# Kernel optimization log

Measured on AMD Instinct MI355X. Metric: run time of the kernel, lower is better.

The kernel has to match this reference:

```python
import jax, jax.numpy as jnp
import numpy as np

# dims: S slots, B batch, D pred-rep dim, E slot-embedding dim, H hidden/output dim, V per-slot vocab
S, B, D, E, H, V = 7, 4096, 1024, 128, 512, 200
D0 = D + E  # layer-0 LSTM input size


def setup_inputs() -> dict:
    key = jax.random.key(0)
    ks = jax.random.split(key, 12)
    rn = lambda k, shape, s=0.02: jax.random.normal(k, shape, jnp.float32) * s
    return {
        "pred_reps": jax.random.normal(ks[0], (B, D), jnp.float32),
        "slot_labels": jax.random.randint(ks[1], (S, B), 0, V),
        "emb": rn(ks[2], (S, V, E), 1.0),
        # layer 0: per-slot LSTMCell + highway params
        "Wih0": rn(ks[3], (S, 4 * H, D0)), "Whh0": rn(ks[4], (S, 4 * H, H)),
        "bih0": jnp.zeros((S, 4 * H), jnp.float32), "bhh0": jnp.zeros((S, 4 * H), jnp.float32),
        "hwW0": rn(ks[5], (S, H, D0 + H)), "hwb0": jnp.zeros((S, H), jnp.float32),
        "linW0": rn(ks[6], (S, H, D0)),
        # layer 1 (input size = H)
        "Wih1": rn(ks[7], (S, 4 * H, H)), "Whh1": rn(ks[8], (S, 4 * H, H)),
        "bih1": jnp.zeros((S, 4 * H), jnp.float32), "bhh1": jnp.zeros((S, 4 * H), jnp.float32),
        "hwW1": rn(ks[9], (S, H, 2 * H)), "hwb1": jnp.zeros((S, H), jnp.float32),
        "linW1": rn(ks[10], (S, H, H)),
    }


def _lstm_cell(x, h, c, Wih, Whh, bih, bhh):
    # torch LSTMCell: gates ordered i, f, g, o
    gates = x @ Wih.T + bih + h @ Whh.T + bhh
    i, f, g, o = jnp.split(gates, 4, axis=-1)
    c_new = jax.nn.sigmoid(f) * c + jax.nn.sigmoid(i) * jnp.tanh(g)
    h_new = jax.nn.sigmoid(o) * jnp.tanh(c_new)
    return h_new, c_new


def reference(pred_reps, slot_labels, emb, Wih0, Whh0, bih0, bhh0, hwW0, hwb0, linW0,
              Wih1, Whh1, bih1, bhh1, hwW1, hwb1, linW1):
    def step(carry, xs):
        h0, c0, h1, c1 = carry
        (tbl, idx, wih0, whh0, bi0, bh0, hw0, hb0, lw0,
         wih1, whh1, bi1, bh1, hw1, hb1, lw1) = xs
        # per-slot embedding gather + concat with predicate reps  -> [B, D0]
        x = jnp.concatenate([pred_reps, tbl[idx]], axis=-1)
        # layer 0 cell + highway gate
        h0n, c0n = _lstm_cell(x, h0, c0, wih0, whh0, bi0, bh0)
        gate0 = jax.nn.sigmoid(jnp.concatenate([x, h0n], axis=-1) @ hw0.T + hb0)
        x1 = gate0 * h0n + (1.0 - gate0) * (x @ lw0.T)
        # layer 1 cell (its highway output is dead code in the original: curr_input
        # after the last layer is discarded, so we skip it -- same math)
        h1n, c1n = _lstm_cell(x1, h1, c1, wih1, whh1, bi1, bh1)
        return (h0n, c0n, h1n, c1n), None

    init = tuple(jnp.zeros((B, H), pred_reps.dtype) for _ in range(4))
    xs = (emb, slot_labels, Wih0, Whh0, bih0, bhh0, hwW0, hwb0, linW0,
          Wih1, Whh1, bih1, bhh1, hwW1, hwb1, linW1)
    carry, _ = jax.lax.scan(step, init, xs)
    return carry[2]  # last_h: top-layer hidden after final slot
```

## Files before the change

kernel.cpp:

```cpp
#include <hip/hip_runtime.h>
#include <stdint.h>

typedef unsigned short u16;

#define S_   7
#define B_   4096
#define D_   1024
#define E_   128
#define H_   512
#define V_   200
#define D0_  1152
#define K0_  1664
#define KX1  1024
#define G4H  2048
#define XW   2048
#define X1W  2048

typedef __bf16 bf16x8 __attribute__((ext_vector_type(8)));
typedef float  f32x4  __attribute__((ext_vector_type(4)));
typedef u16    u16x8  __attribute__((ext_vector_type(8)));

__device__ __forceinline__ u16 f2bf(float f) {
  union { float f; uint32_t u; } v; v.f = f;
  uint32_t r = v.u + 0x7fffu + ((v.u >> 16) & 1u);
  return (u16)(r >> 16);
}
__device__ __forceinline__ float bf2f(u16 b) {
  union { uint32_t u; float f; } v; v.u = ((uint32_t)b) << 16;
  return v.f;
}
__device__ __forceinline__ float sigmoidf_(float x) { return 1.0f / (1.0f + __expf(-x)); }
__device__ __forceinline__ float tanhf_(float x) {
  float t = __expf(-2.f * fabsf(x));
  return copysignf((1.f - t) / (1.f + t), x);
}

__device__ __forceinline__ void glds16(const u16* g, u16* l) {
  __builtin_amdgcn_global_load_lds(
      (const __attribute__((address_space(1))) uint32_t*)g,
      (__attribute__((address_space(3))) uint32_t*)l, 16, 0, 0);
}

__device__ __forceinline__ void cvt8s(const float* src, u16* dst) {
  const float4* p = (const float4*)src;
  float4 x = p[0], y = p[1];
  u16x8 o;
  o[0]=f2bf(x.x); o[1]=f2bf(x.y); o[2]=f2bf(x.z); o[3]=f2bf(x.w);
  o[4]=f2bf(y.x); o[5]=f2bf(y.y); o[6]=f2bf(y.z); o[7]=f2bf(y.w);
  *(u16x8*)dst = o;
}

__device__ __forceinline__ void pk_gates(const float* __restrict__ Wih,
                                         const float* __restrict__ Whh,
                                         u16* __restrict__ dst,
                                         int idx, int stride, int NG, int KK,
                                         int P1, int P2, int KA, int KB) {
  #pragma unroll
  for (int u = 0; u < 4; ++u) {
    int i = idx + u * stride;
    int r = i / NG, kg = i - r * NG;
    int k8 = kg * 8;
    int g = r >> 9, j = r & 511;
    long drow = (j >> 4) * 64 + g * 16 + (j & 15);
    const float* sp = (k8 < P1) ? Wih + (long)r * KA + k8
                    : (k8 < P2) ? Whh + (long)r * KB + (k8 - P1)
                                : Wih + (long)r * KA + P1 + (k8 - P2);
    cvt8s(sp, &dst[drow * KK + k8]);
  }
}
__device__ __forceinline__ void pk_hw(const float* __restrict__ src,
                                      u16* __restrict__ dst,
                                      int idx, int stride, int off16, int KS, bool Z2) {
  #pragma unroll
  for (int u = 0; u < 4; ++u) {
    int i = idx + u * stride;
    int r = i / 208, kg = i - r * 208;
    int k8 = kg * 8;
    long drow = ((r & 511) >> 4) * 32 + off16 + (r & 15);
    u16* d = &dst[drow * K0_ + k8];
    if (Z2 && k8 >= 1024 && k8 < 1536) {
      u16x8 z = {};
      *(u16x8*)d = z;
    } else {
      const float* sp = (k8 < 1024) ? src + (long)r * KS + k8
                      : (k8 < 1536) ? src + (long)r * KS + 1152 + (k8 - 1024)
                                    : src + (long)r * KS + 1024 + (k8 - 1536);
      cvt8s(sp, d);
    }
  }
}

__global__ void pack_predz4(const float* __restrict__ pred, u16* __restrict__ dst) {
  const int NG = XW / 8;
  const int stride = gridDim.x * 256;
  int idx = blockIdx.x * 256 + threadIdx.x;
  #pragma unroll
  for (int u = 0; u < 4; ++u) {
    int i = idx + u * stride;
    int row = i / NG, kg = i - row * NG;
    int k8 = kg * 8;
    u16* d = &dst[(long)row * XW + k8];
    if (k8 < 1024) {
      cvt8s(pred + (long)row * D_ + k8, d);
    } else {
      u16x8 z = {};
      *(u16x8*)d = z;
    }
  }
}

__global__ void xgather(const float* __restrict__ emb, const int* __restrict__ labels,
                        u16* __restrict__ EMB) {
  int b = blockIdx.x;
  int e = threadIdx.x;
  #pragma unroll
  for (int s = 0; s < S_; ++s) {
    int ix = labels[s * B_ + b];
    EMB[((long)(s * B_ + b)) * E_ + e] = f2bf(emb[((long)(s * V_ + ix)) * E_ + e]);
  }
}

__global__ void bias_sum(const float* __restrict__ a, const float* __restrict__ b,
                         float* __restrict__ o, int n) {
  int i = blockIdx.x * 256 + threadIdx.x;
  if (i < n) o[i] = a[i] + b[i];
}
__global__ void zero_f(float* __restrict__ p, int n) {
  for (int i = blockIdx.x * 256 + threadIdx.x; i < n; i += gridDim.x * 256) p[i] = 0.f;
}
__global__ void zero_u16k(u16* __restrict__ p, int n) {
  for (int i = blockIdx.x * 256 + threadIdx.x; i < n; i += gridDim.x * 256) p[i] = 0;
}

struct GemmP {
  const u16 *r0, *r1, *r2, *W;
  const float *bsum;
  float *cbuf;
  u16 *hdst;
  float *hf32;
  const u16 *h0src;
  int ld0, ld1, ld2, t1, t2, ldw, nt, ntn, tnw_sh, ncc_sh, tmw, hld, hoff, h0ld, mode;
};
struct PackP {
  const float *wih0, *whh0, *wih1, *whh1, *hww, *linw;
  u16 *wc0, *wc1, *whl;
};

__global__ __launch_bounds__(256, 4)
void gemm_multi(GemmP pa, GemmP pb, GemmP pc, PackP pk, int nA, int nAB, int nABC) {
  const int b   = blockIdx.x;
  const int tid = threadIdx.x;

  if (b >= nABC) {
    int rb = b - nABC;
    if (rb < 416) {
      pk_gates(pk.wih0, pk.whh0, pk.wc0, rb * 256 + tid, 416 * 256,
               208, K0_, 1024, 1536, D0_, H_);
    } else if (rb < 672) {
      pk_gates(pk.wih1, pk.whh1, pk.wc1, (rb - 416) * 256 + tid, 256 * 256,
               128, KX1, 512, 1024, H_, H_);
    } else {
      int sb = rb - 672;
      if (sb < 104) pk_hw(pk.hww,  pk.whl, sb * 256 + tid,        104 * 256, 0,  K0_, false);
      else          pk_hw(pk.linw, pk.whl, (sb - 104) * 256 + tid, 104 * 256, 16, D0_, true);
    }
    return;
  }

  __shared__ __align__(16) u16 lds[4 * 4096];
  GemmP P = pc; int base = nAB;
  if (b < nAB) { P = pb; base = nA; }
  if (b < nA)  { P = pa; base = 0; }
  const int bidx = b - base;

  u16* lA = lds;
  u16* lW = lds + 2 * 4096;
  const int lane = tid & 63;
  const int wave = tid >> 6;
  const int xcd = bidx & 7, ci = bidx >> 3;
  const int tn = ((xcd & ((1 << P.ncc_sh) - 1)) << P.tnw_sh) | (ci & ((1 << P.tnw_sh) - 1));
  const int tm = (xcd >> P.ncc_sh) * P.tmw + (ci >> P.tnw_sh);
  const long row0 = (long)tm * 128;
  const long col0 = (long)tn * 128;
  const int wm = (wave >> 1) * 64;
  const int wn = (wave & 1) * 64;
  const int fr = lane & 15;
  const int hi = lane >> 4;

  const int s_row = wave * 16 + (lane >> 2);
  const int scol = ((lane & 3) ^ ((lane >> 3) & 3)) * 8;
  const u16* gr0 = P.r0 + (row0 + s_row) * (long)P.ld0 + scol;
  const u16* gr1 = P.r1 + (row0 + s_row) * (long)P.ld1 + scol;
  const u16* gr2 = P.r2 + (row0 + s_row) * (long)P.ld2 + scol;
  const u16* gw  = P.W  + (col0 + s_row) * (long)P.ldw + scol;
  const int dst0 = wave * 512 + lane * 8;

  auto stage = [&](int t, int buf) {
    const u16* g; long ld;
    if (t < P.t1)      { g = gr0 + (long)t * 32;          ld = P.ld0; }
    else if (t < P.t2) { g = gr1 + (long)(t - P.t1) * 32; ld = P.ld1; }
    else               { g = gr2 + (long)(t - P.t2) * 32; ld = P.ld2; }
    const u16* gww = gw + (long)t * 32;
    u16* dA = lA + buf * 4096 + dst0;
    u16* dW = lW + buf * 4096 + dst0;
    glds16(g,           dA);
    glds16(g + 64 * ld, dA + 2048);
    glds16(gww,                      dW);
    glds16(gww + 64 * (long)P.ldw,   dW + 2048);
  };

  const int koff = (hi ^ ((fr >> 1) & 3)) * 8;
  int aoff[4], woff[4];
  #pragma unroll
  for (int m = 0; m < 4; ++m) aoff[m] = (wm + m * 16 + fr) * 32 + koff;
  #pragma unroll
  for (int n = 0; n < 4; ++n) woff[n] = (wn + n * 16 + fr) * 32 + koff;

  f32x4 acc[4][4] = {};
  const int nt = P.nt;

  stage(0, 0);

  for (int t = 0; t < nt; ++t) {
    __syncthreads();
    if (t + 1 < nt) stage(t + 1, (t + 1) & 1);
    const u16* Ab = lA + (t & 1) * 4096;
    const u16* Wb = lW + (t & 1) * 4096;
    bf16x8 af[4], wf[4];
    #pragma unroll
    for (int m = 0; m < 4; ++m) af[m] = *(const bf16x8*)&Ab[aoff[m]];
    #pragma unroll
    for (int n = 0; n < 4; ++n) wf[n] = *(const bf16x8*)&Wb[woff[n]];
    #pragma unroll
    for (int m = 0; m < 4; ++m)
      #pragma unroll
      for (int n = 0; n < 4; ++n)
        acc[m][n] = __builtin_amdgcn_mfma_f32_16x16x32_bf16(af[m], wf[n], acc[m][n], 0, 0, 0);
  }

  const int cr = (lane >> 4) * 4;
  const int jg = wn >> 6;

  if (P.mode == 0) {
    const int j = tn * 32 + jg * 16 + fr;
    const float bi = P.bsum[j], bf = P.bsum[512 + j];
    const float bg = P.bsum[1024 + j], bo = P.bsum[1536 + j];
    #pragma unroll
    for (int m = 0; m < 4; ++m) {
      const long rbase = row0 + wm + m * 16 + cr;
      #pragma unroll
      for (int r = 0; r < 4; ++r) {
        const long ri = rbase + r;
        float gi = acc[m][0][r] + bi;
        float gf = acc[m][1][r] + bf;
        float gg = acc[m][2][r] + bg;
        float go = acc[m][3][r] + bo;
        float cv = P.cbuf[ri * H_ + j];
        float cn = sigmoidf_(gf) * cv + sigmoidf_(gi) * tanhf_(gg);
        float hn = sigmoidf_(go) * tanhf_(cn);
        P.cbuf[ri * H_ + j] = cn;
        P.hdst[ri * P.hld + P.hoff + j] = f2bf(hn);
        if (P.hf32) P.hf32[ri * H_ + j] = hn;
      }
    }
  } else {
    #pragma unroll
    for (int pp = 0; pp < 2; ++pp) {
      const int j = tn * 64 + jg * 32 + pp * 16 + fr;
      const float bj = P.bsum[j];
      #pragma unroll
      for (int m = 0; m < 4; ++m) {
        const long rbase = row0 + wm + m * 16 + cr;
        #pragma unroll
        for (int r = 0; r < 4; ++r) {
          const long ri = rbase + r;
          float gv = sigmoidf_(acc[m][2 * pp][r] + bj);
          float h0 = bf2f(P.h0src[ri * (long)P.h0ld + j]);
          float x1 = gv * h0 + (1.f - gv) * acc[m][2 * pp + 1][r];
          P.hdst[ri * P.hld + P.hoff + j] = f2bf(x1);
        }
      }
    }
  }
}

extern "C" void kernel_launch(void* const* d_in, const int* in_sizes, int n_in,
                              void* d_out, int out_size, void* d_ws, size_t ws_size,
                              hipStream_t stream) {
  const float* pred   = (const float*)d_in[0];
  const int*   labels = (const int*)d_in[1];
  const float* emb    = (const float*)d_in[2];
  const float* Wih0   = (const float*)d_in[3];
  const float* Whh0   = (const float*)d_in[4];
  const float* bih0   = (const float*)d_in[5];
  const float* bhh0   = (const float*)d_in[6];
  const float* hwW0   = (const float*)d_in[7];
  const float* hwb0   = (const float*)d_in[8];
  const float* linW0  = (const float*)d_in[9];
  const float* Wih1   = (const float*)d_in[10];
  const float* Whh1   = (const float*)d_in[11];
  const float* bih1   = (const float*)d_in[12];
  const float* bhh1   = (const float*)d_in[13];
  float* out = (float*)d_out;

  char* ws = (char*)d_ws;
  size_t off = 0;
  auto alloc = [&](size_t bytes) {
    char* p = ws + off;
    off = (off + bytes + 255) & ~(size_t)255;
    return p;
  };
  u16* WC0   = (u16*)alloc((size_t)S_ * G4H * K0_ * 2);
  u16* WHLw  = (u16*)alloc((size_t)S_ * 1024 * K0_ * 2);
  u16* WC1   = (u16*)alloc((size_t)S_ * G4H * KX1 * 2);
  u16* xcat  = (u16*)alloc((size_t)B_ * XW * 2);
  u16* EMB   = (u16*)alloc((size_t)S_ * B_ * E_ * 2);
  u16* x1cat = (u16*)alloc((size_t)B_ * X1W * 2);
  float* c0   = (float*)alloc((size_t)B_ * H_ * 4);
  float* c1   = (float*)alloc((size_t)B_ * H_ * 4);
  float* bs0  = (float*)alloc((size_t)S_ * G4H * 4);
  float* bs1  = (float*)alloc((size_t)S_ * G4H * 4);

  auto mkPk = [&](int s) {
    PackP K;
    K.wih0 = Wih0 + (size_t)s * G4H * D0_;
    K.whh0 = Whh0 + (size_t)s * G4H * H_;
    K.wih1 = Wih1 + (size_t)s * G4H * H_;
    K.whh1 = Whh1 + (size_t)s * G4H * H_;
    K.hww  = hwW0 + (size_t)s * H_ * K0_;
    K.linw = linW0 + (size_t)s * H_ * D0_;
    K.wc0  = WC0  + (size_t)s * G4H * K0_;
    K.wc1  = WC1  + (size_t)s * G4H * KX1;
    K.whl  = WHLw + (size_t)s * 1024 * K0_;
    return K;
  };

  GemmP z = {};
  gemm_multi<<<880, 256, 0, stream>>>(z, z, z, mkPk(0), 0, 0, 0);
  pack_predz4<<<1024, 256, 0, stream>>>(pred, xcat);
  xgather<<<B_, E_, 0, stream>>>(emb, labels, EMB);
  bias_sum<<<56, 256, 0, stream>>>(bih0, bhh0, bs0, S_ * G4H);
  bias_sum<<<56, 256, 0, stream>>>(bih1, bhh1, bs1, S_ * G4H);
  zero_f<<<256, 256, 0, stream>>>(c0, B_ * H_);
  zero_f<<<256, 256, 0, stream>>>(c1, B_ * H_);
  zero_u16k<<<2048, 256, 0, stream>>>(x1cat, B_ * X1W);

  auto mkA = [&](int s) {
    GemmP P;
    P.r0 = xcat;                               P.ld0 = XW;  P.t1 = 32;
    P.r1 = xcat + 1024 + ((s + 1) & 1) * 512;  P.ld1 = XW;  P.t2 = 48;
    P.r2 = EMB + (size_t)s * B_ * E_;          P.ld2 = E_;
    P.W = WC0 + (size_t)s * G4H * K0_;         P.ldw = K0_; P.nt = 52;
    P.ntn = 16; P.tnw_sh = 3; P.ncc_sh = 1; P.tmw = 8;
    P.bsum = bs0 + (size_t)s * G4H; P.cbuf = c0;
    P.hdst = xcat; P.hld = XW; P.hoff = 1024 + (s & 1) * 512;
    P.hf32 = nullptr; P.h0src = xcat; P.h0ld = 0; P.mode = 0;
    return P;
  };
  auto mkB = [&](int s) {
    GemmP P;
    P.r0 = xcat;                               P.ld0 = XW;  P.t1 = 32;
    P.r1 = xcat + 1024 + (s & 1) * 512;        P.ld1 = XW;  P.t2 = 48;
    P.r2 = EMB + (size_t)s * B_ * E_;          P.ld2 = E_;
    P.W = WHLw + (size_t)s * 1024 * K0_;       P.ldw = K0_; P.nt = 52;
    P.ntn = 8; P.tnw_sh = 2; P.ncc_sh = 1; P.tmw = 8;
    P.bsum = hwb0 + (size_t)s * H_; P.cbuf = nullptr;
    P.hdst = x1cat; P.hld = X1W; P.hoff = (s & 1) * 512;
    P.hf32 = nullptr;
    P.h0src = xcat + 1024 + (s & 1) * 512; P.h0ld = XW; P.mode = 1;
    return P;
  };
  auto mkC = [&](int s) {
    GemmP P;
    P.r0 = x1cat + (s & 1) * 512;              P.ld0 = X1W; P.t1 = 16;
    P.r1 = x1cat + 1024 + ((s + 1) & 1) * 512; P.ld1 = X1W; P.t2 = 32;
    P.r2 = P.r0;                               P.ld2 = X1W;
    P.W = WC1 + (size_t)s * G4H * KX1;         P.ldw = KX1; P.nt = 32;
    P.ntn = 16; P.tnw_sh = 3; P.ncc_sh = 1; P.tmw = 8;
    P.bsum = bs1 + (size_t)s * G4H; P.cbuf = c1;
    P.hdst = x1cat; P.hld = X1W; P.hoff = 1024 + (s & 1) * 512;
    P.hf32 = (s == 6) ? out : nullptr; P.h0src = x1cat; P.h0ld = 0; P.mode = 0;
    return P;
  };

  for (int k = 0; k <= 8; ++k) {
    const int nA = (k <= 6) ? 512 : 0;
    const int nB = (k >= 1 && k <= 7) ? 256 : 0;
    const int nC = (k >= 2) ? 512 : 0;
    const int nD = (k <= 5) ? 880 : 0;
    GemmP pa, pb, pc;
    if (nA) pa = mkA(k);
    if (nB) pb = mkB(k - 1);
    if (nC) pc = mkC(k - 2);
    GemmP any = nA ? pa : (nB ? pb : pc);
    if (!nA) pa = any;
    if (!nB) pb = any;
    if (!nC) pc = any;
    PackP pk = mkPk(nD ? (k + 1) : 0);
    gemm_multi<<<nA + nB + nC + nD, 256, 0, stream>>>(pa, pb, pc, pk,
                                                      nA, nA + nB, nA + nB + nC);
  }
}
```

Before: 657.2 us.

## Enlarge GEMM tiles to 256x128 with BK=64 and triple-buffered LDS pipeline

The fused GEMM kernel moves to 512-thread blocks, each computing a 256x128 output tile with a K step of 64 instead of 32. LDS now holds three buffers, and the mainloop uses explicit vmcnt waits so two stages stay in flight. MFMA issue is wrapped in s_setprio. The aim is more data reuse per LDS load and fewer barriers per K-element. The cost is a large LDS footprint (about 147KB per block), which probably limits each CU to one resident block and lowers occupancy. Grid sizes and the weight-pack block partitioning are rescaled to match.

```diff
diff --git a/kernel.cpp b/kernel.cpp
--- a/kernel.cpp
+++ b/kernel.cpp
@@ -146,96 +146,114 @@
   u16 *wc0, *wc1, *whl;
 };
 
-__global__ __launch_bounds__(256, 4)
+__global__ __launch_bounds__(512, 2)
 void gemm_multi(GemmP pa, GemmP pb, GemmP pc, PackP pk, int nA, int nAB, int nABC) {
   const int b   = blockIdx.x;
   const int tid = threadIdx.x;
 
   if (b >= nABC) {
     int rb = b - nABC;
-    if (rb < 416) {
-      pk_gates(pk.wih0, pk.whh0, pk.wc0, rb * 256 + tid, 416 * 256,
+    if (rb < 208) {
+      pk_gates(pk.wih0, pk.whh0, pk.wc0, rb * 512 + tid, 208 * 512,
                208, K0_, 1024, 1536, D0_, H_);
-    } else if (rb < 672) {
-      pk_gates(pk.wih1, pk.whh1, pk.wc1, (rb - 416) * 256 + tid, 256 * 256,
+    } else if (rb < 336) {
+      pk_gates(pk.wih1, pk.whh1, pk.wc1, (rb - 208) * 512 + tid, 128 * 512,
                128, KX1, 512, 1024, H_, H_);
+    } else if (rb < 388) {
+      pk_hw(pk.hww,  pk.whl, (rb - 336) * 512 + tid, 52 * 512, 0,  K0_, false);
     } else {
-      int sb = rb - 672;
-      if (sb < 104) pk_hw(pk.hww,  pk.whl, sb * 256 + tid,        104 * 256, 0,  K0_, false);
-      else          pk_hw(pk.linw, pk.whl, (sb - 104) * 256 + tid, 104 * 256, 16, D0_, true);
+      pk_hw(pk.linw, pk.whl, (rb - 388) * 512 + tid, 52 * 512, 16, D0_, true);
     }
     return;
   }
 
-  __shared__ __align__(16) u16 lds[4 * 4096];
+  __shared__ __align__(16) u16 lds[3 * 16384 + 3 * 8192];
+  u16* lA = lds;
+  u16* lW = lds + 3 * 16384;
+
   GemmP P = pc; int base = nAB;
   if (b < nAB) { P = pb; base = nA; }
   if (b < nA)  { P = pa; base = 0; }
   const int bidx = b - base;
 
-  u16* lA = lds;
-  u16* lW = lds + 2 * 4096;
   const int lane = tid & 63;
   const int wave = tid >> 6;
   const int xcd = bidx & 7, ci = bidx >> 3;
   const int tn = ((xcd & ((1 << P.ncc_sh) - 1)) << P.tnw_sh) | (ci & ((1 << P.tnw_sh) - 1));
   const int tm = (xcd >> P.ncc_sh) * P.tmw + (ci >> P.tnw_sh);
-  const long row0 = (long)tm * 128;
+  const long row0 = (long)tm * 256;
   const long col0 = (long)tn * 128;
   const int wm = (wave >> 1) * 64;
   const int wn = (wave & 1) * 64;
   const int fr = lane & 15;
-  const int hi = lane >> 4;
-
-  const int s_row = wave * 16 + (lane >> 2);
-  const int scol = ((lane & 3) ^ ((lane >> 3) & 3)) * 8;
-  const u16* gr0 = P.r0 + (row0 + s_row) * (long)P.ld0 + scol;
-  const u16* gr1 = P.r1 + (row0 + s_row) * (long)P.ld1 + scol;
-  const u16* gr2 = P.r2 + (row0 + s_row) * (long)P.ld2 + scol;
-  const u16* gw  = P.W  + (col0 + s_row) * (long)P.ldw + scol;
+  const int fk = (lane >> 4) * 8;
+
+  const int srow = wave * 8 + (lane >> 3);
+  const int scol = ((lane & 7) ^ ((lane >> 3) & 7)) * 8;
+  const u16* gr0 = P.r0 + (row0 + srow) * (long)P.ld0 + scol;
+  const u16* gr1 = P.r1 + (row0 + srow) * (long)P.ld1 + scol;
+  const u16* gr2 = P.r2 + (row0 + srow) * (long)P.ld2 + scol;
+  const u16* gw  = P.W  + (col0 + srow) * (long)P.ldw + scol;
   const int dst0 = wave * 512 + lane * 8;
 
   auto stage = [&](int t, int buf) {
     const u16* g; long ld;
-    if (t < P.t1)      { g = gr0 + (long)t * 32;          ld = P.ld0; }
-    else if (t < P.t2) { g = gr1 + (long)(t - P.t1) * 32; ld = P.ld1; }
-    else               { g = gr2 + (long)(t - P.t2) * 32; ld = P.ld2; }
-    const u16* gww = gw + (long)t * 32;
-    u16* dA = lA + buf * 4096 + dst0;
-    u16* dW = lW + buf * 4096 + dst0;
-    glds16(g,           dA);
-    glds16(g + 64 * ld, dA + 2048);
-    glds16(gww,                      dW);
-    glds16(gww + 64 * (long)P.ldw,   dW + 2048);
-  };
-
-  const int koff = (hi ^ ((fr >> 1) & 3)) * 8;
+    if (t < P.t1)      { g = gr0 + (long)t * 64;          ld = P.ld0; }
+    else if (t < P.t2) { g = gr1 + (long)(t - P.t1) * 64; ld = P.ld1; }
+    else               { g = gr2 + (long)(t - P.t2) * 64; ld = P.ld2; }
+    const u16* gww = gw + (long)t * 64;
+    u16* dA = lA + buf * 16384 + dst0;
+    u16* dW = lW + buf * 8192 + dst0;
+    #pragma unroll
+    for (int i = 0; i < 4; ++i) glds16(g + (long)(i * 64) * ld, dA + i * 4096);
+    #pragma unroll
+    for (int j2 = 0; j2 < 2; ++j2) glds16(gww + (long)(j2 * 64) * P.ldw, dW + j2 * 4096);
+  };
+
   int aoff[4], woff[4];
   #pragma unroll
-  for (int m = 0; m < 4; ++m) aoff[m] = (wm + m * 16 + fr) * 32 + koff;
-  #pragma unroll
-  for (int n = 0; n < 4; ++n) woff[n] = (wn + n * 16 + fr) * 32 + koff;
+  for (int m = 0; m < 4; ++m) aoff[m] = (wm + m * 16 + fr) * 64;
+  #pragma unroll
+  for (int n = 0; n < 4; ++n) woff[n] = (wn + n * 16 + fr) * 64;
+  const int swz = (fr & 7) << 3;
+  const int kk0 = (0 + fk) ^ swz;
+  const int kk1 = (32 + fk) ^ swz;
 
   f32x4 acc[4][4] = {};
   const int nt = P.nt;
 
   stage(0, 0);
+  stage(1, 1);
 
   for (int t = 0; t < nt; ++t) {
-    __syncthreads();
-    if (t + 1 < nt) stage(t + 1, (t + 1) & 1);
-    const u16* Ab = lA + (t & 1) * 4096;
-    const u16* Wb = lW + (t & 1) * 4096;
-    bf16x8 af[4], wf[4];
-    #pragma unroll
-    for (int m = 0; m < 4; ++m) af[m] = *(const bf16x8*)&Ab[aoff[m]];
-    #pragma unroll
-    for (int n = 0; n < 4; ++n) wf[n] = *(const bf16x8*)&Wb[woff[n]];
+    if (t + 1 < nt) asm volatile("s_waitcnt vmcnt(6)\n\ts_barrier" ::: "memory");
+    else            asm volatile("s_waitcnt vmcnt(0)\n\ts_barrier" ::: "memory");
+    if (t + 2 < nt) stage(t + 2, (t + 2) % 3);
+
+    const u16* Ab = lA + (t % 3) * 16384;
+    const u16* Wb = lW + (t % 3) * 8192;
+    bf16x8 af0[4], wf0[4], af1[4], wf1[4];
+    #pragma unroll
+    for (int m = 0; m < 4; ++m) af0[m] = *(const bf16x8*)&Ab[aoff[m] + kk0];
+    #pragma unroll
+    for (int n = 0; n < 4; ++n) wf0[n] = *(const bf16x8*)&Wb[woff[n] + kk0];
+    #pragma unroll
+    for (int m = 0; m < 4; ++m) af1[m] = *(const bf16x8*)&Ab[aoff[m] + kk1];
+    #pragma unroll
+    for (int n = 0; n < 4; ++n) wf1[n] = *(const bf16x8*)&Wb[woff[n] + kk1];
+
+    __builtin_amdgcn_s_setprio(1);
     #pragma unroll
     for (int m = 0; m < 4; ++m)
       #pragma unroll
       for (int n = 0; n < 4; ++n)
-        acc[m][n] = __builtin_amdgcn_mfma_f32_16x16x32_bf16(af[m], wf[n], acc[m][n], 0, 0, 0);
+        acc[m][n] = __builtin_amdgcn_mfma_f32_16x16x32_bf16(af0[m], wf0[n], acc[m][n], 0, 0, 0);
+    #pragma unroll
+    for (int m = 0; m < 4; ++m)
+      #pragma unroll
+      for (int n = 0; n < 4; ++n)
+        acc[m][n] = __builtin_amdgcn_mfma_f32_16x16x32_bf16(af1[m], wf1[n], acc[m][n], 0, 0, 0);
+    __builtin_amdgcn_s_setprio(0);
   }
 
   const int cr = (lane >> 4) * 4;
@@ -336,7 +354,7 @@
   };
 
   GemmP z = {};
-  gemm_multi<<<880, 256, 0, stream>>>(z, z, z, mkPk(0), 0, 0, 0);
+  gemm_multi<<<440, 512, 0, stream>>>(z, z, z, mkPk(0), 0, 0, 0);
   pack_predz4<<<1024, 256, 0, stream>>>(pred, xcat);
   xgather<<<B_, E_, 0, stream>>>(emb, labels, EMB);
   bias_sum<<<56, 256, 0, stream>>>(bih0, bhh0, bs0, S_ * G4H);
@@ -347,11 +365,11 @@
 
   auto mkA = [&](int s) {
     GemmP P;
-    P.r0 = xcat;                               P.ld0 = XW;  P.t1 = 32;
-    P.r1 = xcat + 1024 + ((s + 1) & 1) * 512;  P.ld1 = XW;  P.t2 = 48;
+    P.r0 = xcat;                               P.ld0 = XW;  P.t1 = 16;
+    P.r1 = xcat + 1024 + ((s + 1) & 1) * 512;  P.ld1 = XW;  P.t2 = 24;
     P.r2 = EMB + (size_t)s * B_ * E_;          P.ld2 = E_;
-    P.W = WC0 + (size_t)s * G4H * K0_;         P.ldw = K0_; P.nt = 52;
-    P.ntn = 16; P.tnw_sh = 3; P.ncc_sh = 1; P.tmw = 8;
+    P.W = WC0 + (size_t)s * G4H * K0_;         P.ldw = K0_; P.nt = 26;
+    P.ntn = 16; P.tnw_sh = 3; P.ncc_sh = 1; P.tmw = 4;
     P.bsum = bs0 + (size_t)s * G4H; P.cbuf = c0;
     P.hdst = xcat; P.hld = XW; P.hoff = 1024 + (s & 1) * 512;
     P.hf32 = nullptr; P.h0src = xcat; P.h0ld = 0; P.mode = 0;
@@ -359,11 +377,11 @@
   };
   auto mkB = [&](int s) {
     GemmP P;
-    P.r0 = xcat;                               P.ld0 = XW;  P.t1 = 32;
-    P.r1 = xcat + 1024 + (s & 1) * 512;        P.ld1 = XW;  P.t2 = 48;
+    P.r0 = xcat;                               P.ld0 = XW;  P.t1 = 16;
+    P.r1 = xcat + 1024 + (s & 1) * 512;        P.ld1 = XW;  P.t2 = 24;
     P.r2 = EMB + (size_t)s * B_ * E_;          P.ld2 = E_;
-    P.W = WHLw + (size_t)s * 1024 * K0_;       P.ldw = K0_; P.nt = 52;
-    P.ntn = 8; P.tnw_sh = 2; P.ncc_sh = 1; P.tmw = 8;
+    P.W = WHLw + (size_t)s * 1024 * K0_;       P.ldw = K0_; P.nt = 26;
+    P.ntn = 8; P.tnw_sh = 2; P.ncc_sh = 1; P.tmw = 4;
     P.bsum = hwb0 + (size_t)s * H_; P.cbuf = nullptr;
     P.hdst = x1cat; P.hld = X1W; P.hoff = (s & 1) * 512;
     P.hf32 = nullptr;
@@ -372,11 +390,11 @@
   };
   auto mkC = [&](int s) {
     GemmP P;
-    P.r0 = x1cat + (s & 1) * 512;              P.ld0 = X1W; P.t1 = 16;
-    P.r1 = x1cat + 1024 + ((s + 1) & 1) * 512; P.ld1 = X1W; P.t2 = 32;
+    P.r0 = x1cat + (s & 1) * 512;              P.ld0 = X1W; P.t1 = 8;
+    P.r1 = x1cat + 1024 + ((s + 1) & 1) * 512; P.ld1 = X1W; P.t2 = 16;
     P.r2 = P.r0;                               P.ld2 = X1W;
-    P.W = WC1 + (size_t)s * G4H * KX1;         P.ldw = KX1; P.nt = 32;
-    P.ntn = 16; P.tnw_sh = 3; P.ncc_sh = 1; P.tmw = 8;
+    P.W = WC1 + (size_t)s * G4H * KX1;         P.ldw = KX1; P.nt = 16;
+    P.ntn = 16; P.tnw_sh = 3; P.ncc_sh = 1; P.tmw = 4;
     P.bsum = bs1 + (size_t)s * G4H; P.cbuf = c1;
     P.hdst = x1cat; P.hld = X1W; P.hoff = 1024 + (s & 1) * 512;
     P.hf32 = (s == 6) ? out : nullptr; P.h0src = x1cat; P.h0ld = 0; P.mode = 0;
@@ -384,10 +402,10 @@
   };
 
   for (int k = 0; k <= 8; ++k) {
-    const int nA = (k <= 6) ? 512 : 0;
-    const int nB = (k >= 1 && k <= 7) ? 256 : 0;
-    const int nC = (k >= 2) ? 512 : 0;
-    const int nD = (k <= 5) ? 880 : 0;
+    const int nA = (k <= 6) ? 256 : 0;
+    const int nB = (k >= 1 && k <= 7) ? 128 : 0;
+    const int nC = (k >= 2) ? 256 : 0;
+    const int nD = (k <= 5) ? 440 : 0;
     GemmP pa, pb, pc;
     if (nA) pa = mkA(k);
     if (nB) pb = mkB(k - 1);
@@ -397,7 +415,7 @@
     if (!nB) pb = any;
     if (!nC) pc = any;
     PackP pk = mkPk(nD ? (k + 1) : 0);
-    gemm_multi<<<nA + nB + nC + nD, 256, 0, stream>>>(pa, pb, pc, pk,
+    gemm_multi<<<nA + nB + nC + nD, 512, 0, stream>>>(pa, pb, pc, pk,
                                                       nA, nA + nB, nA + nB + nC);
   }
 }
```

New measurement: 626.6 us. 1.05x faster.
